# Optimization experiments

Hardware: AMD Instinct MI355X
Metric: run time of the kernel (lower is better)

Reference implementation:

```python
import jax, jax.numpy as jnp
import numpy as np

B, T, DIN, DH, DE, C = 32, 256, 768, 512, 25, 9


def _xavier(k, shape):
    lim = float(np.sqrt(6.0 / (shape[0] + shape[1])))
    return jax.random.uniform(k, shape, jnp.float32, -lim, lim)


def _unif(k, shape, s):
    return jax.random.uniform(k, shape, jnp.float32, -s, s)


def setup_inputs() -> dict:
    key = jax.random.key(0)
    ks = jax.random.split(key, 14)
    s = 1.0 / float(np.sqrt(DH))
    return {
        "X": jax.random.normal(ks[0], (B, T, DIN), jnp.float32),
        "pad": _xavier(ks[1], (1, DIN)),
        "label_emb": _xavier(ks[2], (C + 1, DE)),
        "Wih_f": _unif(ks[3], (3 * DH, 3 * DIN), s),
        "Whh_f": _unif(ks[4], (3 * DH, DH), s),
        "bih_f": _unif(ks[5], (3 * DH,), s),
        "bhh_f": _unif(ks[6], (3 * DH,), s),
        "Wih_b": _unif(ks[7], (3 * DH, 3 * DIN), s),
        "Whh_b": _unif(ks[8], (3 * DH, DH), s),
        "bih_b": _unif(ks[9], (3 * DH,), s),
        "bhh_b": _unif(ks[10], (3 * DH,), s),
        "Wc": _unif(ks[11], (C, 2 * DH + DE), 1.0 / float(np.sqrt(2 * DH + DE))),
        "bc": _unif(ks[12], (C,), 1.0 / float(np.sqrt(2 * DH + DE))),
    }


def _gru_dir(x, Wih, Whh, bih, bhh, reverse):
    # x: [B, T, 3*DIN]; torch GRU gate order r, z, n
    def step(h, xt):
        gi = xt @ Wih.T + bih              # [B, 3H]
        gh = h @ Whh.T + bhh               # [B, 3H]
        ir, iz, i_n = jnp.split(gi, 3, axis=1)
        hr, hz, h_n = jnp.split(gh, 3, axis=1)
        r = jax.nn.sigmoid(ir + hr)
        z = jax.nn.sigmoid(iz + hz)
        n = jnp.tanh(i_n + r * h_n)
        h = (1.0 - z) * n + z * h
        return h, h
    h0 = jnp.zeros((x.shape[0], Whh.shape[1]), x.dtype)
    _, ys = jax.lax.scan(step, h0, jnp.swapaxes(x, 0, 1), reverse=reverse)
    return jnp.swapaxes(ys, 0, 1)          # [B, T, H]


def reference(X, pad, label_emb, Wih_f, Whh_f, bih_f, bhh_f, Wih_b, Whh_b, bih_b, bhh_b, Wc, bc):
    b = X.shape[0]
    pad_b = jnp.broadcast_to(pad[None, :, :], (b, 1, X.shape[2]))
    X_pad = jnp.concatenate([pad_b, X, pad_b], axis=1)       # [B, T+2, DIN]
    lmr = jnp.concatenate([X_pad[:, :-2, :], X_pad[:, 1:-1, :], X_pad[:, 2:, :]], axis=2)  # [B, T, 3*DIN]
    out_f = _gru_dir(lmr, Wih_f, Whh_f, bih_f, bhh_f, False)
    out_b = _gru_dir(lmr, Wih_b, Whh_b, bih_b, bhh_b, True)
    output_h = jnp.concatenate([out_f, out_b], axis=2)       # [B, T, 2*DH]

    n_labels = label_emb.shape[0] - 1  # start token = last row

    def dec_step(prev, ht):
        # prev: [B] int32 label indices; ht: [B, 2*DH]
        hi = jnp.concatenate([ht, label_emb[prev]], axis=1)   # [B, 2*DH + DE]
        logits = hi @ Wc.T + bc
        probs = jax.nn.softmax(logits, axis=1)
        return jnp.argmax(logits, axis=1).astype(jnp.int32), probs

    prev0 = jnp.full((b,), n_labels, dtype=jnp.int32)
    _, probs_t = jax.lax.scan(dec_step, prev0, jnp.swapaxes(output_h, 0, 1))  # [T, B, C]
    output_chunk = jnp.swapaxes(probs_t, 0, 1).reshape(-1, Wc.shape[0])       # [B*T, C]
    return output_h, output_chunk
```

## Files before the change

kernel.cpp:

```cpp
#include <hip/hip_runtime.h>
#include <hip/hip_bf16.h>
#include <math.h>

#define Bn   32
#define Tn   256
#define DIN  768
#define DHn  512
#define DEn  25
#define Cn   9
#define K3   2304
#define H3   1536
#define NCOL 3072
#define MROW 8192

typedef __attribute__((ext_vector_type(8))) short short8v;
typedef __attribute__((ext_vector_type(4))) float f32x4;

__device__ __forceinline__ unsigned short f2bf(float v) {
  __hip_bfloat16 h = __float2bfloat16(v);
  return __builtin_bit_cast(unsigned short, h);
}
__device__ __forceinline__ float bf2f(unsigned short u) {
  return __bfloat162float(__builtin_bit_cast(__hip_bfloat16, u));
}

#define GBM 128
#define GBN 128
#define GBK 32
#define ASTR 40

__global__ __launch_bounds__(256) void gi_gemm_mfma_kernel(
    const float* __restrict__ X, const float* __restrict__ pad,
    const float* __restrict__ Wf, const float* __restrict__ Wb,
    const float* __restrict__ bf, const float* __restrict__ bb,
    float* __restrict__ gi)
{
  __shared__ __align__(16) unsigned short Ah[GBM * ASTR];
  __shared__ __align__(16) unsigned short Al[GBM * ASTR];
  __shared__ __align__(16) unsigned short Bh[GBN * ASTR];
  __shared__ __align__(16) unsigned short Bl[GBN * ASTR];

  const int bnb = blockIdx.x;
  const int bmb = blockIdx.y;
  const int tid = threadIdx.x;
  const int m0 = bmb * GBM, n0 = bnb * GBN;
  const bool isF = (n0 < H3);
  const float* Wmat = isF ? Wf : Wb;
  const float* bias = isF ? bf : bb;
  const int nb0 = isF ? n0 : (n0 - H3);

  const int r = tid >> 1, half = tid & 1;
  const int m = m0 + r;
  const int ab = m >> 8, tpos = m & 255;
  const float* wrowp = Wmat + (size_t)(nb0 + r) * K3;

  const int wave = tid >> 6, lane = tid & 63;
  const int wr = wave >> 1, wc = wave & 1;
  const int lrow = lane & 15, lk = (lane >> 4) * 8;

  f32x4 acc[4][4];
#pragma unroll
  for (int i = 0; i < 4; i++)
#pragma unroll
    for (int j = 0; j < 4; j++) acc[i][j] = (f32x4){0.f, 0.f, 0.f, 0.f};

  for (int k0 = 0; k0 < K3; k0 += GBK) {
#pragma unroll
    for (int j2 = 0; j2 < 2; j2++) {
      const int kg = k0 + half * 16 + j2 * 8;
      const int seg = (kg >= DIN) + (kg >= 2 * DIN);
      const int off = kg - seg * DIN;
      const int p = tpos + seg;
      const float* srcA = (p == 0 || p == Tn + 1)
                            ? (pad + off)
                            : (X + (size_t)(ab * Tn + (p - 1)) * DIN + off);
      float4 a0 = *reinterpret_cast<const float4*>(srcA);
      float4 a1 = *reinterpret_cast<const float4*>(srcA + 4);
      const float* srcB = wrowp + kg;
      float4 b0 = *reinterpret_cast<const float4*>(srcB);
      float4 b1 = *reinterpret_cast<const float4*>(srcB + 4);

      float av[8] = {a0.x, a0.y, a0.z, a0.w, a1.x, a1.y, a1.z, a1.w};
      float bv[8] = {b0.x, b0.y, b0.z, b0.w, b1.x, b1.y, b1.z, b1.w};
      short8v ah8, al8, bh8, bl8;
#pragma unroll
      for (int q = 0; q < 8; q++) {
        unsigned short h = f2bf(av[q]);
        ah8[q] = (short)h;
        al8[q] = (short)f2bf(av[q] - bf2f(h));
        unsigned short g = f2bf(bv[q]);
        bh8[q] = (short)g;
        bl8[q] = (short)f2bf(bv[q] - bf2f(g));
      }
      const int si = r * ASTR + half * 16 + j2 * 8;
      *reinterpret_cast<short8v*>(&Ah[si]) = ah8;
      *reinterpret_cast<short8v*>(&Al[si]) = al8;
      *reinterpret_cast<short8v*>(&Bh[si]) = bh8;
      *reinterpret_cast<short8v*>(&Bl[si]) = bl8;
    }
    __syncthreads();

    short8v fah[4], fal[4], fbh[4], fbl[4];
#pragma unroll
    for (int i = 0; i < 4; i++) {
      const int ai = (wr * 64 + i * 16 + lrow) * ASTR + lk;
      const int bi = (wc * 64 + i * 16 + lrow) * ASTR + lk;
      fah[i] = *reinterpret_cast<const short8v*>(&Ah[ai]);
      fal[i] = *reinterpret_cast<const short8v*>(&Al[ai]);
      fbh[i] = *reinterpret_cast<const short8v*>(&Bh[bi]);
      fbl[i] = *reinterpret_cast<const short8v*>(&Bl[bi]);
    }
#pragma unroll
    for (int mi = 0; mi < 4; mi++)
#pragma unroll
      for (int ni = 0; ni < 4; ni++) {
        acc[mi][ni] = __builtin_amdgcn_mfma_f32_16x16x32_bf16(fah[mi], fbh[ni], acc[mi][ni], 0, 0, 0);
        acc[mi][ni] = __builtin_amdgcn_mfma_f32_16x16x32_bf16(fah[mi], fbl[ni], acc[mi][ni], 0, 0, 0);
        acc[mi][ni] = __builtin_amdgcn_mfma_f32_16x16x32_bf16(fal[mi], fbh[ni], acc[mi][ni], 0, 0, 0);
      }
    __syncthreads();
  }

#pragma unroll
  for (int ni = 0; ni < 4; ni++) {
    const int nl = wc * 64 + ni * 16 + (lane & 15);
    const float bvv = bias[nb0 + nl];
#pragma unroll
    for (int mi = 0; mi < 4; mi++) {
      const int mg = m0 + wr * 64 + mi * 16 + (lane >> 4) * 4;
#pragma unroll
      for (int reg = 0; reg < 4; reg++)
        gi[(size_t)(mg + reg) * NCOL + n0 + nl] = acc[mi][ni][reg] + bvv;
    }
  }
}

__global__ __launch_bounds__(256) void prep_kernel(
    const float* __restrict__ Whh_f, const float* __restrict__ Whh_b,
    float4* __restrict__ Wp, unsigned* __restrict__ sync)
{
  int f = blockIdx.x * 256 + threadIdx.x;
  if (f < 8) sync[f * 32] = 0u;
  if (f >= 2 * 32 * 16 * 512) return;
  int k   = f & 511;
  int u   = (f >> 9) & 15;
  int slc = (f >> 13) & 31;
  int d   = f >> 18;
  const float* Wsrc = d ? Whh_b : Whh_f;
  int ug = slc * 16 + u;
  float4 v;
  v.x = Wsrc[(size_t)(0 * DHn + ug) * DHn + k];
  v.y = Wsrc[(size_t)(1 * DHn + ug) * DHn + k];
  v.z = Wsrc[(size_t)(2 * DHn + ug) * DHn + k];
  v.w = 0.f;
  Wp[f] = v;
}

__global__ __launch_bounds__(128) void etab_kernel(
    const float* __restrict__ label_emb, const float* __restrict__ Wc,
    float* __restrict__ etab)
{
  int t = threadIdx.x;
  if (t >= 90) return;
  int p = t / Cn, c = t % Cn;
  float a = 0.f;
#pragma unroll
  for (int j = 0; j < DEn; j++)
    a = fmaf(label_emb[p * DEn + j], Wc[(size_t)c * 1049 + 1024 + j], a);
  etab[t] = a;
}

#define HSTRIDE 12

__global__ __launch_bounds__(256) void gru_rec4_kernel(
    const float* __restrict__ gi,
    const float4* __restrict__ Wp,
    const float* __restrict__ bhh_f, const float* __restrict__ bhh_b,
    unsigned* __restrict__ sync,
    float* __restrict__ hex,
    float* __restrict__ out)
{
  __shared__ __align__(16) float4 Wl[16 * 512];
  __shared__ __align__(16) float hl[512 * HSTRIDE];

  const int bid = blockIdx.x;
  const int xcd = bid & 7;
  const int d = xcd >> 2, g = xcd & 3;
  const int sl = bid >> 3;
  const int tid = threadIdx.x;
  const int ut = tid >> 4;
  const int kq = tid & 15;
  const int grp = d * 4 + g;

  {
    const float4* src = Wp + (size_t)(d * 32 + sl) * 8192;
    for (int i = tid; i < 8192; i += 256) Wl[i] = src[i];
  }
  for (int i = tid; i < 512 * HSTRIDE; i += 256) hl[i] = 0.f;

  const float* bhh = d ? bhh_b : bhh_f;
  const int ug = sl * 16 + ut;
  const float br = bhh[ug], bz = bhh[DHn + ug], bn2 = bhh[2 * DHn + ug];
  const int b_l = ((kq & 1) << 2) | (kq & 2) | ((kq >> 2) & 1);

  unsigned* cnt = sync + grp * 32;

  __syncthreads();

  for (int s = 0; s < Tn; s++) {
    const int t = d ? (Tn - 1 - s) : s;

    float ir = 0.f, iz = 0.f, inn = 0.f;
    if (kq < 8) {
      const int bg = g * 8 + b_l;
      const float* gp = gi + (size_t)(bg * Tn + t) * NCOL + d * H3 + ug;
      ir = gp[0]; iz = gp[DHn]; inn = gp[2 * DHn];
    }

    if (s > 0) {
      if (tid == 0) {
        const unsigned tgt = 32u * (unsigned)s;
        while (__hip_atomic_load(cnt, __ATOMIC_RELAXED, __HIP_MEMORY_SCOPE_SYSTEM) < tgt)
          __builtin_amdgcn_s_sleep(1);
      }
      __syncthreads();
      asm volatile("" ::: "memory");
      const uint64_t* src = reinterpret_cast<const uint64_t*>(
          hex + (size_t)(((s - 1) & 1) * 8 + grp) * (512 * 8));
#pragma unroll
      for (int j = 0; j < 8; j++) {
        uint64_t v = __hip_atomic_load(src + tid + 256 * j,
                                       __ATOMIC_RELAXED, __HIP_MEMORY_SCOPE_SYSTEM);
        int fd = 2 * (tid + 256 * j);
        int u = fd >> 3, b = fd & 7;
        *reinterpret_cast<uint64_t*>(&hl[u * HSTRIDE + b]) = v;
      }
      __syncthreads();
    }

    float acc[3][8];
#pragma unroll
    for (int gg = 0; gg < 3; gg++)
#pragma unroll
      for (int bb = 0; bb < 8; bb++) acc[gg][bb] = 0.f;

#pragma unroll 4
    for (int i = 0; i < 32; i++) {
      int k = i * 16 + kq;
      float4 wv = Wl[ut * 512 + k];
      const float* hp = &hl[k * HSTRIDE];
      float4 ha = *reinterpret_cast<const float4*>(hp);
      float4 hb = *reinterpret_cast<const float4*>(hp + 4);
      acc[0][0] = fmaf(wv.x, ha.x, acc[0][0]); acc[0][1] = fmaf(wv.x, ha.y, acc[0][1]);
      acc[0][2] = fmaf(wv.x, ha.z, acc[0][2]); acc[0][3] = fmaf(wv.x, ha.w, acc[0][3]);
      acc[0][4] = fmaf(wv.x, hb.x, acc[0][4]); acc[0][5] = fmaf(wv.x, hb.y, acc[0][5]);
      acc[0][6] = fmaf(wv.x, hb.z, acc[0][6]); acc[0][7] = fmaf(wv.x, hb.w, acc[0][7]);
      acc[1][0] = fmaf(wv.y, ha.x, acc[1][0]); acc[1][1] = fmaf(wv.y, ha.y, acc[1][1]);
      acc[1][2] = fmaf(wv.y, ha.z, acc[1][2]); acc[1][3] = fmaf(wv.y, ha.w, acc[1][3]);
      acc[1][4] = fmaf(wv.y, hb.x, acc[1][4]); acc[1][5] = fmaf(wv.y, hb.y, acc[1][5]);
      acc[1][6] = fmaf(wv.y, hb.z, acc[1][6]); acc[1][7] = fmaf(wv.y, hb.w, acc[1][7]);
      acc[2][0] = fmaf(wv.z, ha.x, acc[2][0]); acc[2][1] = fmaf(wv.z, ha.y, acc[2][1]);
      acc[2][2] = fmaf(wv.z, ha.z, acc[2][2]); acc[2][3] = fmaf(wv.z, ha.w, acc[2][3]);
      acc[2][4] = fmaf(wv.z, hb.x, acc[2][4]); acc[2][5] = fmaf(wv.z, hb.y, acc[2][5]);
      acc[2][6] = fmaf(wv.z, hb.z, acc[2][6]); acc[2][7] = fmaf(wv.z, hb.w, acc[2][7]);
    }

#pragma unroll
    for (int gg = 0; gg < 3; gg++)
#pragma unroll
      for (int bb = 0; bb < 8; bb++)
        acc[gg][bb] += __shfl_xor(acc[gg][bb], 8);

    float a4[3][4];
#pragma unroll
    for (int gg = 0; gg < 3; gg++)
#pragma unroll
      for (int j = 0; j < 4; j++) {
        float keep = (kq & 1) ? acc[gg][4 + j] : acc[gg][j];
        float send = (kq & 1) ? acc[gg][j] : acc[gg][4 + j];
        a4[gg][j] = keep + __shfl_xor(send, 1);
      }
    float a2[3][2];
#pragma unroll
    for (int gg = 0; gg < 3; gg++)
#pragma unroll
      for (int j = 0; j < 2; j++) {
        float keep = (kq & 2) ? a4[gg][2 + j] : a4[gg][j];
        float send = (kq & 2) ? a4[gg][j] : a4[gg][2 + j];
        a2[gg][j] = keep + __shfl_xor(send, 2);
      }
    float a1[3];
#pragma unroll
    for (int gg = 0; gg < 3; gg++) {
      float keep = (kq & 4) ? a2[gg][1] : a2[gg][0];
      float send = (kq & 4) ? a2[gg][0] : a2[gg][1];
      a1[gg] = keep + __shfl_xor(send, 4);
    }

    if (kq < 8) {
      const float r = 1.f / (1.f + expf(-(ir + a1[0] + br)));
      const float z = 1.f / (1.f + expf(-(iz + a1[1] + bz)));
      const float n = tanhf(inn + r * (a1[2] + bn2));
      const float hold = hl[ug * HSTRIDE + b_l];
      const float hnew = (1.f - z) * n + z * hold;
      __hip_atomic_store(&hex[((size_t)(s & 1) * 8 + grp) * (512 * 8) + ug * 8 + b_l],
                         hnew, __ATOMIC_RELAXED, __HIP_MEMORY_SCOPE_SYSTEM);
      out[(size_t)((g * 8 + b_l) * Tn + t) * 1024 + d * DHn + ug] = hnew;
    }
    __syncthreads();
    if (s < Tn - 1 && tid == 0)
      __hip_atomic_fetch_add(cnt, 1u, __ATOMIC_RELAXED, __HIP_MEMORY_SCOPE_SYSTEM);
  }
}

__global__ __launch_bounds__(256) void lh_kernel(
    const float* __restrict__ out_h, const float* __restrict__ Wc,
    const float* __restrict__ bc, float* __restrict__ lh)
{
  const int tid = threadIdx.x;
  const int wave = tid >> 6, lane = tid & 63;
#pragma unroll 1
  for (int it = 0; it < 16; it++) {
    const int row = blockIdx.x * 64 + wave * 16 + it;
    const float* hp = out_h + (size_t)row * 1024 + lane * 4;
    float4 hv[4];
#pragma unroll
    for (int j = 0; j < 4; j++) hv[j] = *reinterpret_cast<const float4*>(hp + 256 * j);
    float acc[Cn];
#pragma unroll
    for (int c = 0; c < Cn; c++) {
      const float* wp = Wc + (size_t)c * 1049 + lane * 4;
      float a = 0.f;
#pragma unroll
      for (int j = 0; j < 4; j++) {
        float4 wv = *reinterpret_cast<const float4*>(wp + 256 * j);
        a = fmaf(hv[j].x, wv.x, a); a = fmaf(hv[j].y, wv.y, a);
        a = fmaf(hv[j].z, wv.z, a); a = fmaf(hv[j].w, wv.w, a);
      }
      acc[c] = a;
    }
#pragma unroll
    for (int off = 32; off; off >>= 1)
#pragma unroll
      for (int c = 0; c < Cn; c++) acc[c] += __shfl_xor(acc[c], off);
    if (lane < Cn) lh[(size_t)row * 12 + lane] = acc[lane] + bc[lane];
  }
}

__global__ __launch_bounds__(64) void chain_kernel(
    const float* __restrict__ lh,
    const float* __restrict__ etab,
    float* __restrict__ outc)
{
  __shared__ float et[90];
  const int tid = threadIdx.x;
  if (tid < 90) et[tid] = etab[tid];
  __syncthreads();
  if (tid >= Bn) return;
  const int b = tid;
  const float* base = lh + (size_t)b * Tn * 12;
  float4 A0 = *reinterpret_cast<const float4*>(base);
  float4 A1 = *reinterpret_cast<const float4*>(base + 4);
  float c8 = base[8];
  int prev = Cn;
  for (int t = 0; t < Tn; t++) {
    float4 N0 = {0,0,0,0}, N1 = {0,0,0,0}; float nc8 = 0.f;
    if (t < Tn - 1) {
      const float* nb = base + (size_t)(t + 1) * 12;
      N0 = *reinterpret_cast<const float4*>(nb);
      N1 = *reinterpret_cast<const float4*>(nb + 4);
      nc8 = nb[8];
    }
    float lg[Cn] = {A0.x, A0.y, A0.z, A0.w, A1.x, A1.y, A1.z, A1.w, c8};
    const float* ep = &et[prev * Cn];
#pragma unroll
    for (int c = 0; c < Cn; c++) lg[c] += ep[c];
    float mx = lg[0]; int idx = 0;
#pragma unroll
    for (int c = 1; c < Cn; c++) if (lg[c] > mx) { mx = lg[c]; idx = c; }
    float e[Cn]; float sum = 0.f;
#pragma unroll
    for (int c = 0; c < Cn; c++) { e[c] = expf(lg[c] - mx); sum += e[c]; }
    const float inv = 1.f / sum;
    float* op = outc + ((size_t)b * Tn + t) * Cn;
#pragma unroll
    for (int c = 0; c < Cn; c++) op[c] = e[c] * inv;
    prev = idx;
    A0 = N0; A1 = N1; c8 = nc8;
  }
}

extern "C" void kernel_launch(void* const* d_in, const int* in_sizes, int n_in,
                              void* d_out, int out_size, void* d_ws, size_t ws_size,
                              hipStream_t stream) {
  const float* X      = (const float*)d_in[0];
  const float* pad    = (const float*)d_in[1];
  const float* lemb   = (const float*)d_in[2];
  const float* Wih_f  = (const float*)d_in[3];
  const float* Whh_f  = (const float*)d_in[4];
  const float* bih_f  = (const float*)d_in[5];
  const float* bhh_f  = (const float*)d_in[6];
  const float* Wih_b  = (const float*)d_in[7];
  const float* Whh_b  = (const float*)d_in[8];
  const float* bih_b  = (const float*)d_in[9];
  const float* bhh_b  = (const float*)d_in[10];
  const float* Wc     = (const float*)d_in[11];
  const float* bc     = (const float*)d_in[12];
  float* out = (float*)d_out;

  char* ws = (char*)d_ws;
  float*    gi   = (float*)ws;
  float4*   Wp   = (float4*)(ws + (size_t)MROW * NCOL * 4);
  unsigned* sync = (unsigned*)(ws + (size_t)MROW * NCOL * 4 + 8388608);
  float*    hex  = (float*)(ws + (size_t)MROW * NCOL * 4 + 8388608 + 1024);
  float*    lh   = (float*)ws;
  float*    etab = (float*)(ws + 524288);

  prep_kernel<<<dim3(2048), dim3(256), 0, stream>>>(Whh_f, Whh_b, Wp, sync);
  gi_gemm_mfma_kernel<<<dim3(NCOL / GBN, MROW / GBM), dim3(256), 0, stream>>>(
      X, pad, Wih_f, Wih_b, bih_f, bih_b, gi);
  gru_rec4_kernel<<<dim3(256), dim3(256), 0, stream>>>(gi, Wp, bhh_f, bhh_b, sync, hex, out);
  etab_kernel<<<dim3(1), dim3(128), 0, stream>>>(lemb, Wc, etab);
  lh_kernel<<<dim3(128), dim3(256), 0, stream>>>(out, Wc, bc, lh);
  chain_kernel<<<dim3(1), dim3(64), 0, stream>>>(lh, etab, out + (size_t)MROW * 1024);
}
```

Before: 2.108 ms.

## Double GRU recurrence threads per block and widen GEMM K tile

The recurrent GRU kernel now runs 512 threads per block, and each thread handles 4 batch columns instead of 8. This halves the serial per-step FMA and shuffle-reduction work per thread, at the cost of more waves contending for LDS. The global store of the hidden output is moved after the step-counter increment, so it no longer delays signalling the other blocks. Separately, the input-projection GEMM doubles its K tile to 64 with two inner MFMA sub-steps, which halves barrier count but uses more LDS per block.

```diff
diff --git a/kernel.cpp b/kernel.cpp
--- a/kernel.cpp
+++ b/kernel.cpp
@@ -26,8 +26,8 @@
 
 #define GBM 128
 #define GBN 128
-#define GBK 32
-#define ASTR 40
+#define GBK 64
+#define ASTR 72
 
 __global__ __launch_bounds__(256) void gi_gemm_mfma_kernel(
     const float* __restrict__ X, const float* __restrict__ pad,
@@ -66,8 +66,8 @@
 
   for (int k0 = 0; k0 < K3; k0 += GBK) {
 #pragma unroll
-    for (int j2 = 0; j2 < 2; j2++) {
-      const int kg = k0 + half * 16 + j2 * 8;
+    for (int j2 = 0; j2 < 4; j2++) {
+      const int kg = k0 + half * 32 + j2 * 8;
       const int seg = (kg >= DIN) + (kg >= 2 * DIN);
       const int off = kg - seg * DIN;
       const int p = tpos + seg;
@@ -92,7 +92,7 @@
         bh8[q] = (short)g;
         bl8[q] = (short)f2bf(bv[q] - bf2f(g));
       }
-      const int si = r * ASTR + half * 16 + j2 * 8;
+      const int si = r * ASTR + half * 32 + j2 * 8;
       *reinterpret_cast<short8v*>(&Ah[si]) = ah8;
       *reinterpret_cast<short8v*>(&Al[si]) = al8;
       *reinterpret_cast<short8v*>(&Bh[si]) = bh8;
@@ -100,24 +100,27 @@
     }
     __syncthreads();
 
-    short8v fah[4], fal[4], fbh[4], fbl[4];
-#pragma unroll
-    for (int i = 0; i < 4; i++) {
-      const int ai = (wr * 64 + i * 16 + lrow) * ASTR + lk;
-      const int bi = (wc * 64 + i * 16 + lrow) * ASTR + lk;
-      fah[i] = *reinterpret_cast<const short8v*>(&Ah[ai]);
-      fal[i] = *reinterpret_cast<const short8v*>(&Al[ai]);
-      fbh[i] = *reinterpret_cast<const short8v*>(&Bh[bi]);
-      fbl[i] = *reinterpret_cast<const short8v*>(&Bl[bi]);
-    }
-#pragma unroll
-    for (int mi = 0; mi < 4; mi++)
-#pragma unroll
-      for (int ni = 0; ni < 4; ni++) {
-        acc[mi][ni] = __builtin_amdgcn_mfma_f32_16x16x32_bf16(fah[mi], fbh[ni], acc[mi][ni], 0, 0, 0);
-        acc[mi][ni] = __builtin_amdgcn_mfma_f32_16x16x32_bf16(fah[mi], fbl[ni], acc[mi][ni], 0, 0, 0);
-        acc[mi][ni] = __builtin_amdgcn_mfma_f32_16x16x32_bf16(fal[mi], fbh[ni], acc[mi][ni], 0, 0, 0);
-      }
+#pragma unroll
+    for (int ksub = 0; ksub < 2; ksub++) {
+      short8v fah[4], fal[4], fbh[4], fbl[4];
+#pragma unroll
+      for (int i = 0; i < 4; i++) {
+        const int ai = (wr * 64 + i * 16 + lrow) * ASTR + ksub * 32 + lk;
+        const int bi = (wc * 64 + i * 16 + lrow) * ASTR + ksub * 32 + lk;
+        fah[i] = *reinterpret_cast<const short8v*>(&Ah[ai]);
+        fal[i] = *reinterpret_cast<const short8v*>(&Al[ai]);
+        fbh[i] = *reinterpret_cast<const short8v*>(&Bh[bi]);
+        fbl[i] = *reinterpret_cast<const short8v*>(&Bl[bi]);
+      }
+#pragma unroll
+      for (int mi = 0; mi < 4; mi++)
+#pragma unroll
+        for (int ni = 0; ni < 4; ni++) {
+          acc[mi][ni] = __builtin_amdgcn_mfma_f32_16x16x32_bf16(fah[mi], fbh[ni], acc[mi][ni], 0, 0, 0);
+          acc[mi][ni] = __builtin_amdgcn_mfma_f32_16x16x32_bf16(fah[mi], fbl[ni], acc[mi][ni], 0, 0, 0);
+          acc[mi][ni] = __builtin_amdgcn_mfma_f32_16x16x32_bf16(fal[mi], fbh[ni], acc[mi][ni], 0, 0, 0);
+        }
+    }
     __syncthreads();
   }
 
@@ -172,7 +175,7 @@
 
 #define HSTRIDE 12
 
-__global__ __launch_bounds__(256) void gru_rec4_kernel(
+__global__ __launch_bounds__(512) void gru_rec5_kernel(
     const float* __restrict__ gi,
     const float4* __restrict__ Wp,
     const float* __restrict__ bhh_f, const float* __restrict__ bhh_b,
@@ -188,20 +191,22 @@
   const int d = xcd >> 2, g = xcd & 3;
   const int sl = bid >> 3;
   const int tid = threadIdx.x;
-  const int ut = tid >> 4;
-  const int kq = tid & 15;
+  const int ut = tid >> 5;
+  const int kq2 = tid & 31;
+  const int kq = kq2 & 15, bh = kq2 >> 4;
   const int grp = d * 4 + g;
 
   {
     const float4* src = Wp + (size_t)(d * 32 + sl) * 8192;
-    for (int i = tid; i < 8192; i += 256) Wl[i] = src[i];
-  }
-  for (int i = tid; i < 512 * HSTRIDE; i += 256) hl[i] = 0.f;
+    for (int i = tid; i < 8192; i += 512) Wl[i] = src[i];
+  }
+  for (int i = tid; i < 512 * HSTRIDE; i += 512) hl[i] = 0.f;
 
   const float* bhh = d ? bhh_b : bhh_f;
   const int ug = sl * 16 + ut;
   const float br = bhh[ug], bz = bhh[DHn + ug], bn2 = bhh[2 * DHn + ug];
-  const int b_l = ((kq & 1) << 2) | (kq & 2) | ((kq >> 2) & 1);
+  const int blocal = ((kq & 1) << 1) | ((kq >> 1) & 1);
+  const int b_l = bh * 4 + blocal;
 
   unsigned* cnt = sync + grp * 32;
 
@@ -211,7 +216,7 @@
     const int t = d ? (Tn - 1 - s) : s;
 
     float ir = 0.f, iz = 0.f, inn = 0.f;
-    if (kq < 8) {
+    if (kq < 4) {
       const int bg = g * 8 + b_l;
       const float* gp = gi + (size_t)(bg * Tn + t) * NCOL + d * H3 + ug;
       ir = gp[0]; iz = gp[DHn]; inn = gp[2 * DHn];
@@ -228,88 +233,77 @@
       const uint64_t* src = reinterpret_cast<const uint64_t*>(
           hex + (size_t)(((s - 1) & 1) * 8 + grp) * (512 * 8));
 #pragma unroll
-      for (int j = 0; j < 8; j++) {
-        uint64_t v = __hip_atomic_load(src + tid + 256 * j,
+      for (int j = 0; j < 4; j++) {
+        int idx = tid + 512 * j;
+        uint64_t v = __hip_atomic_load(src + idx,
                                        __ATOMIC_RELAXED, __HIP_MEMORY_SCOPE_SYSTEM);
-        int fd = 2 * (tid + 256 * j);
+        int fd = 2 * idx;
         int u = fd >> 3, b = fd & 7;
         *reinterpret_cast<uint64_t*>(&hl[u * HSTRIDE + b]) = v;
       }
       __syncthreads();
     }
 
-    float acc[3][8];
+    float acc[3][4];
 #pragma unroll
     for (int gg = 0; gg < 3; gg++)
 #pragma unroll
-      for (int bb = 0; bb < 8; bb++) acc[gg][bb] = 0.f;
+      for (int bb = 0; bb < 4; bb++) acc[gg][bb] = 0.f;
 
 #pragma unroll 4
     for (int i = 0; i < 32; i++) {
       int k = i * 16 + kq;
       float4 wv = Wl[ut * 512 + k];
-      const float* hp = &hl[k * HSTRIDE];
-      float4 ha = *reinterpret_cast<const float4*>(hp);
-      float4 hb = *reinterpret_cast<const float4*>(hp + 4);
+      float4 ha = *reinterpret_cast<const float4*>(&hl[k * HSTRIDE + bh * 4]);
       acc[0][0] = fmaf(wv.x, ha.x, acc[0][0]); acc[0][1] = fmaf(wv.x, ha.y, acc[0][1]);
       acc[0][2] = fmaf(wv.x, ha.z, acc[0][2]); acc[0][3] = fmaf(wv.x, ha.w, acc[0][3]);
-      acc[0][4] = fmaf(wv.x, hb.x, acc[0][4]); acc[0][5] = fmaf(wv.x, hb.y, acc[0][5]);
-      acc[0][6] = fmaf(wv.x, hb.z, acc[0][6]); acc[0][7] = fmaf(wv.x, hb.w, acc[0][7]);
       acc[1][0] = fmaf(wv.y, ha.x, acc[1][0]); acc[1][1] = fmaf(wv.y, ha.y, acc[1][1]);
       acc[1][2] = fmaf(wv.y, ha.z, acc[1][2]); acc[1][3] = fmaf(wv.y, ha.w, acc[1][3]);
-      acc[1][4] = fmaf(wv.y, hb.x, acc[1][4]); acc[1][5] = fmaf(wv.y, hb.y, acc[1][5]);
-      acc[1][6] = fmaf(wv.y, hb.z, acc[1][6]); acc[1][7] = fmaf(wv.y, hb.w, acc[1][7]);
       acc[2][0] = fmaf(wv.z, ha.x, acc[2][0]); acc[2][1] = fmaf(wv.z, ha.y, acc[2][1]);
       acc[2][2] = fmaf(wv.z, ha.z, acc[2][2]); acc[2][3] = fmaf(wv.z, ha.w, acc[2][3]);
-      acc[2][4] = fmaf(wv.z, hb.x, acc[2][4]); acc[2][5] = fmaf(wv.z, hb.y, acc[2][5]);
-      acc[2][6] = fmaf(wv.z, hb.z, acc[2][6]); acc[2][7] = fmaf(wv.z, hb.w, acc[2][7]);
     }
 
 #pragma unroll
     for (int gg = 0; gg < 3; gg++)
 #pragma unroll
-      for (int bb = 0; bb < 8; bb++)
+      for (int bb = 0; bb < 4; bb++)
         acc[gg][bb] += __shfl_xor(acc[gg][bb], 8);
 
-    float a4[3][4];
+    float a2[3][2];
 #pragma unroll
     for (int gg = 0; gg < 3; gg++)
 #pragma unroll
-      for (int j = 0; j < 4; j++) {
-        float keep = (kq & 1) ? acc[gg][4 + j] : acc[gg][j];
-        float send = (kq & 1) ? acc[gg][j] : acc[gg][4 + j];
-        a4[gg][j] = keep + __shfl_xor(send, 1);
-      }
-    float a2[3][2];
+      for (int j = 0; j < 2; j++) {
+        float keep = (kq & 1) ? acc[gg][2 + j] : acc[gg][j];
+        float send = (kq & 1) ? acc[gg][j] : acc[gg][2 + j];
+        a2[gg][j] = keep + __shfl_xor(send, 1);
+      }
+    float a1[3];
+#pragma unroll
+    for (int gg = 0; gg < 3; gg++) {
+      float keep = (kq & 2) ? a2[gg][1] : a2[gg][0];
+      float send = (kq & 2) ? a2[gg][0] : a2[gg][1];
+      a1[gg] = keep + __shfl_xor(send, 2);
+    }
 #pragma unroll
     for (int gg = 0; gg < 3; gg++)
-#pragma unroll
-      for (int j = 0; j < 2; j++) {
-        float keep = (kq & 2) ? a4[gg][2 + j] : a4[gg][j];
-        float send = (kq & 2) ? a4[gg][j] : a4[gg][2 + j];
-        a2[gg][j] = keep + __shfl_xor(send, 2);
-      }
-    float a1[3];
-#pragma unroll
-    for (int gg = 0; gg < 3; gg++) {
-      float keep = (kq & 4) ? a2[gg][1] : a2[gg][0];
-      float send = (kq & 4) ? a2[gg][0] : a2[gg][1];
-      a1[gg] = keep + __shfl_xor(send, 4);
-    }
-
-    if (kq < 8) {
+      a1[gg] += __shfl_xor(a1[gg], 4);
+
+    float hnew = 0.f;
+    if (kq < 4) {
       const float r = 1.f / (1.f + expf(-(ir + a1[0] + br)));
       const float z = 1.f / (1.f + expf(-(iz + a1[1] + bz)));
       const float n = tanhf(inn + r * (a1[2] + bn2));
       const float hold = hl[ug * HSTRIDE + b_l];
-      const float hnew = (1.f - z) * n + z * hold;
+      hnew = (1.f - z) * n + z * hold;
       __hip_atomic_store(&hex[((size_t)(s & 1) * 8 + grp) * (512 * 8) + ug * 8 + b_l],
                          hnew, __ATOMIC_RELAXED, __HIP_MEMORY_SCOPE_SYSTEM);
-      out[(size_t)((g * 8 + b_l) * Tn + t) * 1024 + d * DHn + ug] = hnew;
     }
     __syncthreads();
     if (s < Tn - 1 && tid == 0)
       __hip_atomic_fetch_add(cnt, 1u, __ATOMIC_RELAXED, __HIP_MEMORY_SCOPE_SYSTEM);
+    if (kq < 4)
+      out[(size_t)((g * 8 + b_l) * Tn + t) * 1024 + d * DHn + ug] = hnew;
   }
 }
 
@@ -419,7 +413,7 @@
   prep_kernel<<<dim3(2048), dim3(256), 0, stream>>>(Whh_f, Whh_b, Wp, sync);
   gi_gemm_mfma_kernel<<<dim3(NCOL / GBN, MROW / GBM), dim3(256), 0, stream>>>(
       X, pad, Wih_f, Wih_b, bih_f, bih_b, gi);
-  gru_rec4_kernel<<<dim3(256), dim3(256), 0, stream>>>(gi, Wp, bhh_f, bhh_b, sync, hex, out);
+  gru_rec5_kernel<<<dim3(256), dim3(512), 0, stream>>>(gi, Wp, bhh_f, bhh_b, sync, hex, out);
   etab_kernel<<<dim3(1), dim3(128), 0, stream>>>(lemb, Wc, etab);
   lh_kernel<<<dim3(128), dim3(256), 0, stream>>>(out, Wc, bc, lh);
   chain_kernel<<<dim3(1), dim3(64), 0, stream>>>(lh, etab, out + (size_t)MROW * 1024);
```

After: 1.918 ms. -9.0%, faster.
